# Performance work log

Hardware: AMD Instinct MI355X
Metric: run time of the kernel (lower is better)

Reference implementation:

```python
import jax, jax.numpy as jnp
import numpy as np

B, S, DIM, NH, NKV, HD, HID, L, VOCAB = 1, 2048, 1024, 16, 8, 64, 2816, 2, 32000
EPS = 1e-5
SCALE = float(HD) ** 0.5
NEG = -255.0  # mask fill value used by executorch example inputs


def setup_inputs() -> dict:
    key = jax.random.key(0)
    ks = jax.random.split(key, 16)
    sd = 0.02
    def rnd(k, shape):
        return jax.random.normal(k, shape, dtype=jnp.float32) * sd
    # rope tables: precompute_freqs_cis(head_dim, max_seq_len)[: -1] -> [S, HD//2]
    inv = 1.0 / (10000.0 ** (np.arange(0, HD, 2, dtype=np.float32) / HD))
    ang = np.outer(np.arange(S, dtype=np.float32), inv)
    # causal mask [S, S]
    tril = np.tril(np.ones((S, S), dtype=bool))
    mask = np.where(tril, 0.0, NEG).astype(np.float32)
    return {
        "tokens": jax.random.randint(ks[0], (B, S), 0, VOCAB, dtype=jnp.int32),
        "atten_mask": jnp.asarray(mask),
        "freqs_cos": jnp.asarray(np.cos(ang)),
        "freqs_sin": jnp.asarray(np.sin(ang)),
        "tok_emb": rnd(ks[1], (VOCAB, DIM)),
        "wq": rnd(ks[2], (L, DIM, NH * HD)),
        "wk": rnd(ks[3], (L, DIM, NKV * HD)),
        "wv": rnd(ks[4], (L, DIM, NKV * HD)),
        "wo": rnd(ks[5], (L, NH * HD, DIM)),
        "attn_norm_w": jnp.ones((L, DIM), jnp.float32),
        "ffn_norm_w": jnp.ones((L, DIM), jnp.float32),
        "w1": rnd(ks[6], (L, DIM, HID)),
        "w2": rnd(ks[7], (L, HID, DIM)),
        "w3": rnd(ks[8], (L, DIM, HID)),
        "final_norm_w": jnp.ones((DIM,), jnp.float32),
        "out_w": rnd(ks[9], (DIM, VOCAB)),
    }


def _rmsnorm(x, w):
    return x * jax.lax.rsqrt(jnp.mean(x * x, axis=-1, keepdims=True) + EPS) * w


def _rope(x, c, s):
    # faithful to apply_rotary_emb_single: de-interleave, rotate, concat halves
    xr, xi = x[..., ::2], x[..., 1::2]          # [B,S,H,HD/2]
    c = c[None, :, None, :]
    s = s[None, :, None, :]
    return jnp.concatenate([xr * c - xi * s, xr * s + xi * c], axis=-1)


def reference(tokens, atten_mask, freqs_cos, freqs_sin, tok_emb, wq, wk, wv, wo,
              attn_norm_w, ffn_norm_w, w1, w2, w3, final_norm_w, out_w):
    rep = NH // NKV
    h = tok_emb[tokens]                           # [B,S,DIM]
    k_news, v_news = [], []
    for l in range(L):
        x = _rmsnorm(h, attn_norm_w[l])
        q = (x @ wq[l]).reshape(B, S, NH, HD)
        k = (x @ wk[l]).reshape(B, S, NKV, HD)
        v = (x @ wv[l]).reshape(B, S, NKV, HD)
        q = _rope(q, freqs_cos, freqs_sin)
        k = _rope(k, freqs_cos, freqs_sin)
        # GQA: each kv head serves NH//NKV query heads
        kr = jnp.repeat(k, rep, axis=2)           # [B,S,NH,HD]
        vr = jnp.repeat(v, rep, axis=2)
        attn = jnp.einsum('bshd,bthd->bhst', q, kr) / SCALE + atten_mask[None, None]
        p = jax.nn.softmax(attn, axis=-1)
        y = jnp.einsum('bhst,bthd->bshd', p, vr).reshape(B, S, NH * HD)
        h = h + y @ wo[l]
        x = _rmsnorm(h, ffn_norm_w[l])
        h = h + (jax.nn.silu(x @ w1[l]) * (x @ w3[l])) @ w2[l]
        # output_new_cache_only: last-position rotated K and raw V per kv head
        k_news.append(k[:, -1])                   # [B,NKV,HD]
        v_news.append(v[:, -1])
    logits = _rmsnorm(h, final_norm_w) @ out_w    # [B,S,VOCAB]
    return logits, jnp.stack(k_news), jnp.stack(v_news)
```

## Files before the change

### kernel.cpp

```cpp
#include <hip/hip_runtime.h>
#include <hip/hip_bf16.h>

typedef __bf16 bf16x8 __attribute__((ext_vector_type(8)));
typedef float f32x4 __attribute__((ext_vector_type(4)));
typedef unsigned short ushort4v __attribute__((ext_vector_type(4)));
typedef unsigned short ushort8v __attribute__((ext_vector_type(8)));

#define S_LEN 2048
#define DIM 1024
#define NH 16
#define NKV 8
#define HD 64
#define HID 2816
#define LOGITS ((size_t)S_LEN * 32000)

__device__ __forceinline__ unsigned short f2bf(float f) {
    union { float f; unsigned u; } v; v.f = f;
    unsigned r = v.u + 0x7fffu + ((v.u >> 16) & 1u);
    return (unsigned short)(r >> 16);
}
__device__ __forceinline__ float bf2f(unsigned short u) {
    union { unsigned u; float f; } v; v.u = (unsigned)u << 16; return v.f;
}

__device__ __forceinline__ void gload16(const unsigned short* g, unsigned short* l) {
    __builtin_amdgcn_global_load_lds(
        (const __attribute__((address_space(1))) unsigned int*)g,
        (__attribute__((address_space(3))) unsigned int*)l,
        16, 0, 0);
}

union Frag { f32x4 f; bf16x8 h; };

__device__ __forceinline__ f32x4 lds_read_b128(unsigned addr) {
    f32x4 d;
    asm volatile("ds_read_b128 %0, %1" : "=v"(d) : "v"(addr));
    return d;
}

#define BAR()  asm volatile("s_barrier" ::: "memory")
#define WAITV(n) asm volatile("s_waitcnt vmcnt(" #n ")" ::: "memory")
#define LGKM0() do { asm volatile("s_waitcnt lgkmcnt(0)" ::: "memory"); __builtin_amdgcn_sched_barrier(0); } while (0)

__global__ __launch_bounds__(256) void embed_kernel(const int* __restrict__ tokens,
                                                    const float* __restrict__ emb,
                                                    float* __restrict__ h) {
    int s = blockIdx.x;
    int t = tokens[s];
    float4 v = *(const float4*)&emb[(size_t)t * DIM + threadIdx.x * 4];
    *(float4*)&h[(size_t)s * DIM + threadIdx.x * 4] = v;
}

__global__ __launch_bounds__(256) void rmsnorm_kernel(const float* __restrict__ x,
                                                      const float* __restrict__ w,
                                                      unsigned short* __restrict__ out) {
    __shared__ float sred[4];
    int s = blockIdx.x;
    int tid = threadIdx.x;
    float4 v = *(const float4*)&x[(size_t)s * DIM + tid * 4];
    float ss = v.x * v.x + v.y * v.y + v.z * v.z + v.w * v.w;
#pragma unroll
    for (int off = 32; off; off >>= 1) ss += __shfl_down(ss, off);
    if ((tid & 63) == 0) sred[tid >> 6] = ss;
    __syncthreads();
    float tot = sred[0] + sred[1] + sred[2] + sred[3];
    float scale = rsqrtf(tot * (1.0f / DIM) + 1e-5f);
    float4 wv = *(const float4*)&w[tid * 4];
    ushort4v o;
    o[0] = f2bf(v.x * scale * wv.x); o[1] = f2bf(v.y * scale * wv.y);
    o[2] = f2bf(v.z * scale * wv.z); o[3] = f2bf(v.w * scale * wv.w);
    *(ushort4v*)&out[(size_t)s * DIM + tid * 4] = o;
}

__device__ __forceinline__ void tpose_body(const float* __restrict__ in,
                                           unsigned short* __restrict__ out,
                                           int K, int N, int n0, int k0,
                                           int rowMul, int rowOff) {
    __shared__ unsigned short t[64][68];
    int tid = threadIdx.x;
    int tn = tid & 15, tk = tid >> 4;
#pragma unroll
    for (int p = 0; p < 4; ++p) {
        int k = tk + p * 16;
        float4 v = *(const float4*)&in[(size_t)(k0 + k) * N + n0 + tn * 4];
        t[tn * 4 + 0][k] = f2bf(v.x);
        t[tn * 4 + 1][k] = f2bf(v.y);
        t[tn * 4 + 2][k] = f2bf(v.z);
        t[tn * 4 + 3][k] = f2bf(v.w);
    }
    __syncthreads();
    int wk = tid & 15, wn = tid >> 4;
#pragma unroll
    for (int p = 0; p < 4; ++p) {
        int n = wn + p * 16;
        ushort4v v;
        v[0] = t[n][wk * 4]; v[1] = t[n][wk * 4 + 1];
        v[2] = t[n][wk * 4 + 2]; v[3] = t[n][wk * 4 + 3];
        *(ushort4v*)&out[(size_t)(rowMul * (n0 + n) + rowOff) * K + k0 + wk * 4] = v;
    }
}

__global__ __launch_bounds__(256) void transpose_w(const float* __restrict__ in,
                                                   unsigned short* __restrict__ out,
                                                   int K, int N) {
    tpose_body(in, out, K, N, blockIdx.x * 64, blockIdx.y * 64, 1, 0);
}

__global__ __launch_bounds__(256) void transpose_qkv(const float* __restrict__ wq,
                                                     const float* __restrict__ wk,
                                                     const float* __restrict__ wv,
                                                     unsigned short* __restrict__ out) {
    int z = blockIdx.z;
    if (z > 0 && blockIdx.x >= 8) return;
    const float* in = z == 0 ? wq : (z == 1 ? wk : wv);
    int N = z == 0 ? 1024 : 512;
    int rowOff = z == 0 ? 0 : (z == 1 ? 1024 : 1536);
    tpose_body(in, out, DIM, N, blockIdx.x * 64, blockIdx.y * 64, 1, rowOff);
}

__global__ __launch_bounds__(256) void transpose_w13(const float* __restrict__ w1,
                                                     const float* __restrict__ w3,
                                                     unsigned short* __restrict__ out) {
    int z = blockIdx.z;
    tpose_body(z ? w3 : w1, out, DIM, HID, blockIdx.x * 64, blockIdx.y * 64, 2, z);
}

__global__ __launch_bounds__(256) void transpose_vf(const float* __restrict__ qkvf,
                                                    unsigned short* __restrict__ vT,
                                                    float* __restrict__ out, int layer) {
    __shared__ unsigned short t[64][72];
    int c0 = blockIdx.x * 64, s0 = blockIdx.y * 64;
    int tid = threadIdx.x;
    int tc = tid & 15, ts = tid >> 4;
#pragma unroll
    for (int p = 0; p < 4; ++p) {
        int s = ts + p * 16;
        float4 v = *(const float4*)&qkvf[(size_t)(s0 + s) * 2048 + 1536 + c0 + tc * 4];
        t[tc * 4 + 0][s] = f2bf(v.x);
        t[tc * 4 + 1][s] = f2bf(v.y);
        t[tc * 4 + 2][s] = f2bf(v.z);
        t[tc * 4 + 3][s] = f2bf(v.w);
        if (s0 + s == S_LEN - 1) {
            float* vn = out + LOGITS + 2 * (NKV * HD) + (size_t)layer * (NKV * HD) + c0 + tc * 4;
            vn[0] = v.x; vn[1] = v.y; vn[2] = v.z; vn[3] = v.w;
        }
    }
    __syncthreads();
    int ws_ = tid & 15, wc = tid >> 4;
#pragma unroll
    for (int p = 0; p < 4; ++p) {
        int c = wc + p * 16;
        ushort4v v;
        v[0] = t[c][ws_ * 4]; v[1] = t[c][ws_ * 4 + 1];
        v[2] = t[c][ws_ * 4 + 2]; v[3] = t[c][ws_ * 4 + 3];
        *(ushort4v*)&vT[(size_t)(c0 + c) * 2048 + s0 + ws_ * 4] = v;
    }
}

__global__ __launch_bounds__(256) void gemm_tn(const unsigned short* __restrict__ A, int lda,
                                               const unsigned short* __restrict__ Bt,
                                               float* __restrict__ Cf,
                                               unsigned short* __restrict__ Cb,
                                               const float* __restrict__ addsrc,
                                               int N, int K) {
    __shared__ unsigned short As[128 * 64];
    __shared__ unsigned short Bs[128 * 64];
    int tid = threadIdx.x;
    int lane = tid & 63;
    int wid = tid >> 6;
    int wrow = wid >> 1, wcol = wid & 1;
    int lr = lane & 15, lg = lane >> 4;
    const int m0 = blockIdx.x * 128, n0 = blockIdx.y * 128;

    const int col8 = (((lane & 7) ^ ((lane >> 3) & 7)) * 8);
    const unsigned short* aG = A + (size_t)(m0 + wid * 32 + (lane >> 3)) * lda + col8;
    const unsigned short* bG = Bt + (size_t)(n0 + wid * 32 + (lane >> 3)) * K + col8;
    unsigned short* aL = As + wid * 2048;
    unsigned short* bL = Bs + wid * 2048;

    f32x4 acc[4][4] = {};

    for (int k0 = 0; k0 < K; k0 += 64) {
#pragma unroll
        for (int i = 0; i < 4; ++i)
            gload16(aG + (size_t)(i * 8) * lda + k0, aL + i * 512);
#pragma unroll
        for (int i = 0; i < 4; ++i)
            gload16(bG + (size_t)(i * 8) * K + k0, bL + i * 512);
        __syncthreads();
#pragma unroll
        for (int kk = 0; kk < 2; ++kk) {
            const int slot = ((kk * 4 + lg) ^ (lr & 7)) * 8;
            bf16x8 aF[4], bF[4];
#pragma unroll
            for (int mi = 0; mi < 4; ++mi)
                aF[mi] = *(const bf16x8*)&As[(wrow * 64 + mi * 16 + lr) * 64 + slot];
#pragma unroll
            for (int ni = 0; ni < 4; ++ni)
                bF[ni] = *(const bf16x8*)&Bs[(wcol * 64 + ni * 16 + lr) * 64 + slot];
#pragma unroll
            for (int mi = 0; mi < 4; ++mi)
#pragma unroll
                for (int ni = 0; ni < 4; ++ni)
                    acc[mi][ni] = __builtin_amdgcn_mfma_f32_16x16x32_bf16(aF[mi], bF[ni], acc[mi][ni], 0, 0, 0);
        }
        __syncthreads();
    }
#pragma unroll
    for (int mi = 0; mi < 4; ++mi)
#pragma unroll
        for (int ni = 0; ni < 4; ++ni) {
            int row = m0 + wrow * 64 + mi * 16 + lg * 4;
            int col = n0 + wcol * 64 + ni * 16 + lr;
#pragma unroll
            for (int r = 0; r < 4; ++r) {
                size_t idx = (size_t)(row + r) * N + col;
                float v = acc[mi][ni][r];
                if (addsrc) v += addsrc[idx];
                if (Cb) Cb[idx] = f2bf(v);
                else    Cf[idx] = v;
            }
        }
}

__global__ __launch_bounds__(256) void gemm_tn64(const unsigned short* __restrict__ A, int lda,
                                                 const unsigned short* __restrict__ Bt,
                                                 float* __restrict__ Cf,
                                                 unsigned short* __restrict__ Cb,
                                                 const float* __restrict__ addsrc,
                                                 int N, int K) {
    __shared__ unsigned short As[64 * 64];
    __shared__ unsigned short Bs[128 * 64];
    int tid = threadIdx.x;
    int lane = tid & 63;
    int wid = tid >> 6;
    int lr = lane & 15, lg = lane >> 4;
    const int m0 = blockIdx.x * 64, n0 = blockIdx.y * 128;

    const int srow = tid >> 3;
    const int col8 = (((tid & 7) ^ ((tid >> 3) & 7)) * 8);
    const unsigned short* aG = A + (size_t)(m0 + srow) * lda + col8;
    const unsigned short* bG = Bt + (size_t)(n0 + srow) * K + col8;
    unsigned short* aL = As + wid * 512;
    unsigned short* bL = Bs + wid * 512;

    f32x4 acc[4][2] = {};

    for (int k0 = 0; k0 < K; k0 += 64) {
        gload16(aG + k0, aL);
        gload16(aG + (size_t)32 * lda + k0, aL + 2048);
#pragma unroll
        for (int i = 0; i < 4; ++i)
            gload16(bG + (size_t)(i * 32) * K + k0, bL + i * 2048);
        __syncthreads();
#pragma unroll
        for (int kk = 0; kk < 2; ++kk) {
            const int slot = ((kk * 4 + lg) ^ (lr & 7)) * 8;
            bf16x8 aF[4], bF[2];
#pragma unroll
            for (int mi = 0; mi < 4; ++mi)
                aF[mi] = *(const bf16x8*)&As[(mi * 16 + lr) * 64 + slot];
#pragma unroll
            for (int ni = 0; ni < 2; ++ni)
                bF[ni] = *(const bf16x8*)&Bs[(wid * 32 + ni * 16 + lr) * 64 + slot];
#pragma unroll
            for (int mi = 0; mi < 4; ++mi)
#pragma unroll
                for (int ni = 0; ni < 2; ++ni)
                    acc[mi][ni] = __builtin_amdgcn_mfma_f32_16x16x32_bf16(aF[mi], bF[ni], acc[mi][ni], 0, 0, 0);
        }
        __syncthreads();
    }
#pragma unroll
    for (int mi = 0; mi < 4; ++mi)
#pragma unroll
        for (int ni = 0; ni < 2; ++ni) {
            int row = m0 + mi * 16 + lg * 4;
            int col = n0 + wid * 32 + ni * 16 + lr;
#pragma unroll
            for (int r = 0; r < 4; ++r) {
                size_t idx = (size_t)(row + r) * N + col;
                float v = acc[mi][ni][r];
                if (addsrc) v += addsrc[idx];
                if (Cb) Cb[idx] = f2bf(v);
                else    Cf[idx] = v;
            }
        }
}

template<int FUSE>
__global__ __launch_bounds__(512) void gemm8(const unsigned short* __restrict__ A,
                                             const unsigned short* __restrict__ Bt,
                                             float* __restrict__ Cf,
                                             unsigned short* __restrict__ Cb,
                                             int N, int K) {
    __shared__ unsigned short ldsbuf[65536];
    const int NT = K >> 6;
    int tid = threadIdx.x;
    int lane = tid & 63;
    int wid = tid >> 6;
    int wm = wid >> 2, wn = wid & 3;
    int lr = lane & 15, lg = lane >> 4;
    int wl = blockIdx.x * gridDim.y + blockIdx.y;
    const int m0 = (wl & 7) * 256, n0 = (wl >> 3) * 256;

    unsigned lds0 = (unsigned)(size_t)(__attribute__((address_space(3))) unsigned short*)ldsbuf;
    const unsigned xoff = (unsigned)((lg ^ ((lr >> 1) & 3)) * 16);
    const int gsw = (lane & 3) ^ ((lane >> 3) & 3);
    const int srow = wid * 16 + (lane >> 2);

#define STAGE(buf, ab, s, t) do {                                                   \
        const unsigned short* _src = (ab) ? Bt : A;                                 \
        int _r0 = (ab) ? n0 : m0;                                                   \
        unsigned short* _l = ldsbuf + (((buf) * 2 + (ab)) * 2 + (s)) * 8192 + wid * 512; \
        const unsigned short* _g = _src + (size_t)(_r0 + srow) * K + (size_t)(t) * 64 + (s) * 32 + gsw * 8; \
        gload16(_g, _l);                                                            \
        gload16(_g + (size_t)128 * K, _l + 4096);                                   \
    } while (0)

    f32x4 acc[8][4] = {};

    STAGE(0, 0, 0, 0); STAGE(0, 1, 0, 0);
    STAGE(0, 0, 1, 0); STAGE(0, 1, 1, 0);
    STAGE(1, 0, 0, 1); STAGE(1, 1, 0, 1);
    WAITV(8);
    BAR();

    for (int t = 0; t < NT; ++t) {
        int buf = t & 1;
        unsigned aBase = lds0 + (unsigned)(buf * 65536) + (unsigned)((wm * 128 + lr) * 64) + xoff;
        unsigned bBase = lds0 + (unsigned)(buf * 65536 + 32768) + (unsigned)((wn * 64 + lr) * 64) + xoff;
        Frag aF[4], bF[4];
#pragma unroll
        for (int s = 0; s < 2; ++s) {
#pragma unroll
            for (int ni = 0; ni < 4; ++ni)
                bF[ni].f = lds_read_b128(bBase + (unsigned)(s * 16384 + ni * 1024));
#pragma unroll
            for (int mi = 0; mi < 4; ++mi)
                aF[mi].f = lds_read_b128(aBase + (unsigned)(s * 16384 + mi * 1024));
            if (s == 0) { if (t + 1 < NT) STAGE(buf ^ 1, 0, 1, t + 1); }
            else        { if (t + 2 < NT) STAGE(buf,     0, 0, t + 2); }
            BAR();
            LGKM0();
            __builtin_amdgcn_s_setprio(1);
#pragma unroll
            for (int mi = 0; mi < 4; ++mi)
#pragma unroll
                for (int ni = 0; ni < 4; ++ni)
                    acc[mi][ni] = __builtin_amdgcn_mfma_f32_16x16x32_bf16(aF[mi].h, bF[ni].h, acc[mi][ni], 0, 0, 0);
            __builtin_amdgcn_s_setprio(0);
            BAR();
#pragma unroll
            for (int mi = 0; mi < 4; ++mi)
                aF[mi].f = lds_read_b128(aBase + (unsigned)(4096 + s * 16384 + mi * 1024));
            if (s == 0) { if (t + 1 < NT) STAGE(buf ^ 1, 1, 1, t + 1); }
            else        { if (t + 2 < NT) STAGE(buf,     1, 0, t + 2); }
            BAR();
            LGKM0();
            __builtin_amdgcn_s_setprio(1);
#pragma unroll
            for (int mi = 0; mi < 4; ++mi)
#pragma unroll
                for (int ni = 0; ni < 4; ++ni)
                    acc[4 + mi][ni] = __builtin_amdgcn_mfma_f32_16x16x32_bf16(aF[mi].h, bF[ni].h, acc[4 + mi][ni], 0, 0, 0);
            __builtin_amdgcn_s_setprio(0);
            if (s == 0) {
                if (t + 1 < NT) { WAITV(8); } else { WAITV(0); }
            } else {
                if (t + 2 < NT)      { WAITV(8); }
                else if (t + 1 < NT) { WAITV(4); }
            }
            BAR();
        }
    }
#undef STAGE

#pragma unroll
    for (int mi = 0; mi < 8; ++mi)
#pragma unroll
        for (int ni = 0; ni < 4; ++ni) {
            int row = m0 + wm * 128 + mi * 16 + lg * 4;
            int col = n0 + wn * 64 + ni * 16 + lr;
#pragma unroll
            for (int r = 0; r < 4; ++r) {
                float v = acc[mi][ni][r];
                if (FUSE) {
                    float o = __shfl_xor(v, 1);
                    if (!(lr & 1)) {
                        float res = v / (1.f + __expf(-v)) * o;
                        Cb[(size_t)(row + r) * (HID) + (col >> 1)] = f2bf(res);
                    }
                } else {
                    Cf[(size_t)(row + r) * N + col] = v;
                }
            }
        }
}

__global__ __launch_bounds__(256) void rope_kernel(const float* __restrict__ qkv,
                                                   const float* __restrict__ fc,
                                                   const float* __restrict__ fs,
                                                   unsigned short* __restrict__ qb,
                                                   unsigned short* __restrict__ kb,
                                                   float* __restrict__ out, int layer) {
    int s = blockIdx.x * 4 + (threadIdx.x >> 6);
    int hh = blockIdx.y;
    int lane = threadIdx.x & 63;
    if (lane >= 32) return;
    const float* base = qkv + (size_t)s * 2048;
    if (hh < NH) {
        const float* row = base + hh * HD;
        float2 x2 = *(const float2*)&row[2 * lane];
        float c = fc[s * 32 + lane], sn = fs[s * 32 + lane];
        size_t o = (size_t)s * (NH * HD) + hh * HD + lane;
        qb[o] = f2bf(x2.x * c - x2.y * sn);
        qb[o + 32] = f2bf(x2.x * sn + x2.y * c);
    } else {
        int kh = hh - NH;
        const float* row = base + 1024 + kh * HD;
        float2 x2 = *(const float2*)&row[2 * lane];
        float c = fc[s * 32 + lane], sn = fs[s * 32 + lane];
        float o0 = x2.x * c - x2.y * sn, o1 = x2.x * sn + x2.y * c;
        size_t o = (size_t)s * (NKV * HD) + kh * HD + lane;
        kb[o] = f2bf(o0);
        kb[o + 32] = f2bf(o1);
        if (s == S_LEN - 1) {
            float* kn = out + LOGITS + (size_t)layer * (NKV * HD) + kh * HD;
            kn[lane] = o0; kn[lane + 32] = o1;
        }
    }
}

__global__ __launch_bounds__(256) void attn_kernel(const unsigned short* __restrict__ qb,
                                                   const unsigned short* __restrict__ kb,
                                                   const unsigned short* __restrict__ vT,
                                                   unsigned short* __restrict__ yb) {
    __shared__ unsigned short Klds[2][4096];
    __shared__ unsigned short Vlds[2][4096];
    __shared__ unsigned short P[4][16 * 72];
    int kvh = blockIdx.x;
    int strip = 63 - blockIdx.y;
    int tid = threadIdx.x;
    int lane = tid & 63;
    int w = tid >> 6;
    int hq = w & 1, qsub = w >> 1;
    int h = kvh * 2 + hq;
    int lr = lane & 15, lg = lane >> 4;
    int qbase = strip * 32 + qsub * 16;
    int qrow = qbase + lr;

    const int sr = tid >> 3;
    const int scol8 = (((tid & 7) ^ (sr & 7)) * 8);
    const int NT = (strip >> 1) + 1;

#define STAGEKV(buf, kt) do { \
        gload16(&kb[(size_t)((kt) * 64 + sr) * 512 + kvh * 64 + scol8], &Klds[buf][w * 512]); \
        gload16(&kb[(size_t)((kt) * 64 + sr + 32) * 512 + kvh * 64 + scol8], &Klds[buf][2048 + w * 512]); \
        gload16(&vT[(size_t)(kvh * 64 + sr) * 2048 + (kt) * 64 + scol8], &Vlds[buf][w * 512]); \
        gload16(&vT[(size_t)(kvh * 64 + sr + 32) * 2048 + (kt) * 64 + scol8], &Vlds[buf][2048 + w * 512]); \
    } while (0)

    bf16x8 bq[2];
#pragma unroll
    for (int c = 0; c < 2; ++c)
        bq[c] = *(const bf16x8*)&qb[(size_t)qrow * (NH * HD) + h * HD + c * 32 + lg * 8];

    f32x4 O[4] = {};
    float mstate = -1e30f, lstate = 0.f;

    STAGEKV(0, 0);
    WAITV(0);
    BAR();

    for (int kt = 0; kt < NT; ++kt) {
        int buf = kt & 1;
        if (kt + 1 < NT) STAGEKV(buf ^ 1, kt + 1);
        f32x4 s[4];
#pragma unroll
        for (int kc = 0; kc < 4; ++kc) {
            int krl = kc * 16 + lr;
            const unsigned short* kp = &Klds[buf][krl * 64];
            bf16x8 ak0 = *(const bf16x8*)&kp[((lg ^ (lr & 7)) * 8)];
            bf16x8 ak1 = *(const bf16x8*)&kp[(((4 + lg) ^ (lr & 7)) * 8)];
            f32x4 z = {};
            z = __builtin_amdgcn_mfma_f32_16x16x32_bf16(ak0, bq[0], z, 0, 0, 0);
            z = __builtin_amdgcn_mfma_f32_16x16x32_bf16(ak1, bq[1], z, 0, 0, 0);
            s[kc] = z;
        }
        float tm = -1e30f;
#pragma unroll
        for (int kc = 0; kc < 4; ++kc)
#pragma unroll
            for (int r = 0; r < 4; ++r) {
                int key = kt * 64 + kc * 16 + lg * 4 + r;
                float val = s[kc][r] * 0.125f;
                if (key > qrow) val = -1e30f;
                s[kc][r] = val;
                tm = fmaxf(tm, val);
            }
        tm = fmaxf(tm, __shfl_xor(tm, 16));
        tm = fmaxf(tm, __shfl_xor(tm, 32));
        float mn = fmaxf(mstate, tm);
        float sc = __expf(mstate - mn);
        float rs = 0.f;
        ushort4v pk[4];
#pragma unroll
        for (int kc = 0; kc < 4; ++kc)
#pragma unroll
            for (int r = 0; r < 4; ++r) {
                float pf = __expf(s[kc][r] - mn);
                rs += pf;
                pk[kc][r] = f2bf(pf);
            }
        rs += __shfl_xor(rs, 16);
        rs += __shfl_xor(rs, 32);
        lstate = lstate * sc + rs;
        mstate = mn;
        float osc[4];
#pragma unroll
        for (int r = 0; r < 4; ++r)
            osc[r] = __shfl(sc, lg * 4 + r);
#pragma unroll
        for (int n = 0; n < 4; ++n)
#pragma unroll
            for (int r = 0; r < 4; ++r)
                O[n][r] *= osc[r];
#pragma unroll
        for (int kc = 0; kc < 4; ++kc)
            *(ushort4v*)&P[w][lr * 72 + kc * 16 + lg * 4] = pk[kc];
        bf16x8 pa[2];
#pragma unroll
        for (int g = 0; g < 2; ++g)
            pa[g] = *(const bf16x8*)&P[w][lr * 72 + g * 32 + lg * 8];
#pragma unroll
        for (int n = 0; n < 4; ++n) {
            const unsigned short* vp = &Vlds[buf][(n * 16 + lr) * 64];
#pragma unroll
            for (int g = 0; g < 2; ++g) {
                bf16x8 bv = *(const bf16x8*)&vp[(((g * 4 + lg) ^ (lr & 7)) * 8)];
                O[n] = __builtin_amdgcn_mfma_f32_16x16x32_bf16(pa[g], bv, O[n], 0, 0, 0);
            }
        }
        if (kt + 1 < NT) WAITV(0);
        LGKM0();
        BAR();
    }
#undef STAGEKV

    float linv[4];
#pragma unroll
    for (int r = 0; r < 4; ++r)
        linv[r] = 1.f / __shfl(lstate, lg * 4 + r);
#pragma unroll
    for (int n = 0; n < 4; ++n)
#pragma unroll
        for (int r = 0; r < 4; ++r) {
            int row = qbase + lg * 4 + r;
            yb[(size_t)row * (NH * HD) + h * HD + n * 16 + lr] = f2bf(O[n][r] * linv[r]);
        }
}

extern "C" void kernel_launch(void* const* d_in, const int* in_sizes, int n_in,
                              void* d_out, int out_size, void* d_ws, size_t ws_size,
                              hipStream_t stream) {
    const int* tokens = (const int*)d_in[0];
    const float* freqs_cos = (const float*)d_in[2];
    const float* freqs_sin = (const float*)d_in[3];
    const float* tok_emb = (const float*)d_in[4];
    const float* wq = (const float*)d_in[5];
    const float* wk = (const float*)d_in[6];
    const float* wv = (const float*)d_in[7];
    const float* wo = (const float*)d_in[8];
    const float* attn_norm_w = (const float*)d_in[9];
    const float* ffn_norm_w = (const float*)d_in[10];
    const float* w1 = (const float*)d_in[11];
    const float* w2 = (const float*)d_in[12];
    const float* w3 = (const float*)d_in[13];
    const float* final_norm_w = (const float*)d_in[14];
    const float* out_w = (const float*)d_in[15];
    float* out = (float*)d_out;

    const size_t SD = (size_t)S_LEN * DIM;
    const size_t SKV = (size_t)S_LEN * NKV * HD;

    char* p = (char*)d_ws;
    auto take = [&](size_t bytes) { char* r = p; p += (bytes + 255) & ~(size_t)255; return r; };
    float* h            = (float*)take(SD * 4);
    unsigned short* xnb = (unsigned short*)take(SD * 2);
    char* uni = p;
    float* qkvf         = (float*)uni;
    unsigned short* qb  = (unsigned short*)(uni + 17039360);
    unsigned short* kb  = qb + SD;
    unsigned short* vT  = kb + SKV;
    unsigned short* ybv = vT + SKV;
    unsigned short* gu  = ybv + SD;
    unsigned short* wT  = gu + (size_t)S_LEN * HID;
    unsigned short* owT = (unsigned short*)uni;

    embed_kernel<<<S_LEN, 256, 0, stream>>>(tokens, tok_emb, h);
    for (int l = 0; l < 2; ++l) {
        rmsnorm_kernel<<<S_LEN, 256, 0, stream>>>(h, attn_norm_w + l * DIM, xnb);
        transpose_qkv<<<dim3(16, 16, 3), 256, 0, stream>>>(
            wq + (size_t)l * DIM * 1024, wk + (size_t)l * DIM * 512, wv + (size_t)l * DIM * 512, wT);
        gemm_tn<<<dim3(16, 16), 256, 0, stream>>>(xnb, DIM, wT, qkvf, nullptr, nullptr, 2048, DIM);
        rope_kernel<<<dim3(S_LEN / 4, 24), 256, 0, stream>>>(qkvf, freqs_cos, freqs_sin, qb, kb, out, l);
        transpose_vf<<<dim3(8, 32), 256, 0, stream>>>(qkvf, vT, out, l);
        attn_kernel<<<dim3(NKV, 64), 256, 0, stream>>>(qb, kb, vT, ybv);
        transpose_w<<<dim3(16, 16), 256, 0, stream>>>(wo + (size_t)l * 1024 * DIM, wT, 1024, DIM);
        gemm_tn64<<<dim3(32, 8), 256, 0, stream>>>(ybv, 1024, wT, h, nullptr, h, DIM, 1024);
        rmsnorm_kernel<<<S_LEN, 256, 0, stream>>>(h, ffn_norm_w + l * DIM, xnb);
        transpose_w13<<<dim3(44, 16, 2), 256, 0, stream>>>(
            w1 + (size_t)l * DIM * HID, w3 + (size_t)l * DIM * HID, wT);
        gemm8<1><<<dim3(8, 22), 512, 0, stream>>>(xnb, wT, nullptr, gu, 5632, DIM);
        transpose_w<<<dim3(16, 44), 256, 0, stream>>>(w2 + (size_t)l * HID * 1024, wT, HID, 1024);
        gemm_tn64<<<dim3(32, 8), 256, 0, stream>>>(gu, HID, wT, h, nullptr, h, DIM, HID);
    }
    rmsnorm_kernel<<<S_LEN, 256, 0, stream>>>(h, final_norm_w, xnb);
    transpose_w<<<dim3(500, 16), 256, 0, stream>>>(out_w, owT, DIM, 32000);
    gemm8<0><<<dim3(8, 125), 512, 0, stream>>>(xnb, owT, out, nullptr, 32000, DIM);
}
```

Baseline: 669.5 us.

## Fuse RoPE and V transpose into QKV GEMM epilogue; new K32 output GEMM

The QKV projection GEMM now applies rotary embedding in its epilogue, using a lane shuffle to fetch the paired element. It writes bf16 Q/K and transposed V directly, and stores the last-position K/V cache. This removes the fp32 qkvf intermediate and two extra kernel launches (rope and V transpose). Separately, the final vocab projection switches to a new 256x256-tile GEMM with K-step 32, double-buffered direct global-to-LDS loads and raised wave priority around the MFMA blocks. The epilogue stores are scattered, strided 2-byte writes, which may be less efficient than the old coalesced path.

```diff
diff --git a/kernel.cpp b/kernel.cpp
--- a/kernel.cpp
+++ b/kernel.cpp
@@ -125,46 +125,17 @@
     tpose_body(z ? w3 : w1, out, DIM, HID, blockIdx.x * 64, blockIdx.y * 64, 2, z);
 }
 
-__global__ __launch_bounds__(256) void transpose_vf(const float* __restrict__ qkvf,
-                                                    unsigned short* __restrict__ vT,
-                                                    float* __restrict__ out, int layer) {
-    __shared__ unsigned short t[64][72];
-    int c0 = blockIdx.x * 64, s0 = blockIdx.y * 64;
-    int tid = threadIdx.x;
-    int tc = tid & 15, ts = tid >> 4;
-#pragma unroll
-    for (int p = 0; p < 4; ++p) {
-        int s = ts + p * 16;
-        float4 v = *(const float4*)&qkvf[(size_t)(s0 + s) * 2048 + 1536 + c0 + tc * 4];
-        t[tc * 4 + 0][s] = f2bf(v.x);
-        t[tc * 4 + 1][s] = f2bf(v.y);
-        t[tc * 4 + 2][s] = f2bf(v.z);
-        t[tc * 4 + 3][s] = f2bf(v.w);
-        if (s0 + s == S_LEN - 1) {
-            float* vn = out + LOGITS + 2 * (NKV * HD) + (size_t)layer * (NKV * HD) + c0 + tc * 4;
-            vn[0] = v.x; vn[1] = v.y; vn[2] = v.z; vn[3] = v.w;
-        }
-    }
-    __syncthreads();
-    int ws_ = tid & 15, wc = tid >> 4;
-#pragma unroll
-    for (int p = 0; p < 4; ++p) {
-        int c = wc + p * 16;
-        ushort4v v;
-        v[0] = t[c][ws_ * 4]; v[1] = t[c][ws_ * 4 + 1];
-        v[2] = t[c][ws_ * 4 + 2]; v[3] = t[c][ws_ * 4 + 3];
-        *(ushort4v*)&vT[(size_t)(c0 + c) * 2048 + s0 + ws_ * 4] = v;
-    }
-}
-
-__global__ __launch_bounds__(256) void gemm_tn(const unsigned short* __restrict__ A, int lda,
-                                               const unsigned short* __restrict__ Bt,
-                                               float* __restrict__ Cf,
-                                               unsigned short* __restrict__ Cb,
-                                               const float* __restrict__ addsrc,
-                                               int N, int K) {
+__global__ __launch_bounds__(256) void gemm_qkv(const unsigned short* __restrict__ A,
+                                                const unsigned short* __restrict__ Bt,
+                                                const float* __restrict__ fc,
+                                                const float* __restrict__ fs,
+                                                unsigned short* __restrict__ qb,
+                                                unsigned short* __restrict__ kb,
+                                                unsigned short* __restrict__ vT,
+                                                float* __restrict__ out, int layer) {
     __shared__ unsigned short As[128 * 64];
     __shared__ unsigned short Bs[128 * 64];
+    const int K = DIM, lda = DIM;
     int tid = threadIdx.x;
     int lane = tid & 63;
     int wid = tid >> 6;
@@ -210,15 +181,36 @@
     for (int mi = 0; mi < 4; ++mi)
 #pragma unroll
         for (int ni = 0; ni < 4; ++ni) {
-            int row = m0 + wrow * 64 + mi * 16 + lg * 4;
             int col = n0 + wcol * 64 + ni * 16 + lr;
-#pragma unroll
-            for (int r = 0; r < 4; ++r) {
-                size_t idx = (size_t)(row + r) * N + col;
-                float v = acc[mi][ni][r];
-                if (addsrc) v += addsrc[idx];
-                if (Cb) Cb[idx] = f2bf(v);
-                else    Cf[idx] = v;
+            int s0r = m0 + wrow * 64 + mi * 16 + lg * 4;
+            if (col < 1536) {
+                int p = (col & 63) >> 1;
+                int odd = col & 1;
+#pragma unroll
+                for (int r = 0; r < 4; ++r) {
+                    float v = acc[mi][ni][r];
+                    float o = __shfl_xor(v, 1);
+                    int s = s0r + r;
+                    float c = fc[s * 32 + p], sn = fs[s * 32 + p];
+                    float res = odd ? (o * sn + v * c) : (v * c - o * sn);
+                    int dpos = (odd ? 32 : 0) + p;
+                    if (col < 1024) {
+                        qb[(size_t)s * 1024 + (col >> 6) * 64 + dpos] = f2bf(res);
+                    } else {
+                        int kcol = ((col >> 6) - 16) * 64 + dpos;
+                        kb[(size_t)s * 512 + kcol] = f2bf(res);
+                        if (s == S_LEN - 1)
+                            out[LOGITS + (size_t)layer * 512 + kcol] = res;
+                    }
+                }
+            } else {
+                int d = col - 1536;
+                ushort4v vv;
+#pragma unroll
+                for (int r = 0; r < 4; ++r) vv[r] = f2bf(acc[mi][ni][r]);
+                *(ushort4v*)&vT[(size_t)d * 2048 + s0r] = vv;
+                if (s0r + 3 == S_LEN - 1)
+                    out[LOGITS + 2 * 512 + (size_t)layer * 512 + d] = acc[mi][ni][3];
             }
         }
 }
@@ -226,7 +218,6 @@
 __global__ __launch_bounds__(256) void gemm_tn64(const unsigned short* __restrict__ A, int lda,
                                                  const unsigned short* __restrict__ Bt,
                                                  float* __restrict__ Cf,
-                                                 unsigned short* __restrict__ Cb,
                                                  const float* __restrict__ addsrc,
                                                  int N, int K) {
     __shared__ unsigned short As[64 * 64];
@@ -282,8 +273,7 @@
                 size_t idx = (size_t)(row + r) * N + col;
                 float v = acc[mi][ni][r];
                 if (addsrc) v += addsrc[idx];
-                if (Cb) Cb[idx] = f2bf(v);
-                else    Cf[idx] = v;
+                Cf[idx] = v;
             }
         }
 }
@@ -398,38 +388,96 @@
         }
 }
 
-__global__ __launch_bounds__(256) void rope_kernel(const float* __restrict__ qkv,
-                                                   const float* __restrict__ fc,
-                                                   const float* __restrict__ fs,
-                                                   unsigned short* __restrict__ qb,
-                                                   unsigned short* __restrict__ kb,
-                                                   float* __restrict__ out, int layer) {
-    int s = blockIdx.x * 4 + (threadIdx.x >> 6);
-    int hh = blockIdx.y;
-    int lane = threadIdx.x & 63;
-    if (lane >= 32) return;
-    const float* base = qkv + (size_t)s * 2048;
-    if (hh < NH) {
-        const float* row = base + hh * HD;
-        float2 x2 = *(const float2*)&row[2 * lane];
-        float c = fc[s * 32 + lane], sn = fs[s * 32 + lane];
-        size_t o = (size_t)s * (NH * HD) + hh * HD + lane;
-        qb[o] = f2bf(x2.x * c - x2.y * sn);
-        qb[o + 32] = f2bf(x2.x * sn + x2.y * c);
-    } else {
-        int kh = hh - NH;
-        const float* row = base + 1024 + kh * HD;
-        float2 x2 = *(const float2*)&row[2 * lane];
-        float c = fc[s * 32 + lane], sn = fs[s * 32 + lane];
-        float o0 = x2.x * c - x2.y * sn, o1 = x2.x * sn + x2.y * c;
-        size_t o = (size_t)s * (NKV * HD) + kh * HD + lane;
-        kb[o] = f2bf(o0);
-        kb[o + 32] = f2bf(o1);
-        if (s == S_LEN - 1) {
-            float* kn = out + LOGITS + (size_t)layer * (NKV * HD) + kh * HD;
-            kn[lane] = o0; kn[lane + 32] = o1;
-        }
-    }
+__global__ __launch_bounds__(512) void gemm8k32(const unsigned short* __restrict__ A,
+                                                const unsigned short* __restrict__ Bt,
+                                                float* __restrict__ Cf,
+                                                int N, int K) {
+    __shared__ unsigned short ldsbuf[32768];
+    const int NT = K >> 5;
+    int tid = threadIdx.x;
+    int lane = tid & 63;
+    int wid = tid >> 6;
+    int wm = wid >> 2, wn = wid & 3;
+    int lr = lane & 15, lg = lane >> 4;
+    int wl = blockIdx.x * gridDim.y + blockIdx.y;
+    const int m0 = (wl & 7) * 256, n0 = (wl >> 3) * 256;
+
+    unsigned lds0 = (unsigned)(size_t)(__attribute__((address_space(3))) unsigned short*)ldsbuf;
+    const unsigned xoff = (unsigned)((lg ^ ((lr >> 1) & 3)) * 16);
+    const int gsw = (lane & 3) ^ ((lane >> 3) & 3);
+    const int srow = wid * 16 + (lane >> 2);
+
+#define STGA(t) do { \
+        unsigned short* _l = ldsbuf + (((t) & 1) * 2 + 0) * 8192 + wid * 512; \
+        const unsigned short* _g = A + (size_t)(m0 + srow) * K + (size_t)(t) * 32 + gsw * 8; \
+        gload16(_g, _l); \
+        gload16(_g + (size_t)128 * K, _l + 4096); \
+    } while (0)
+#define STGB(t) do { \
+        unsigned short* _l = ldsbuf + (((t) & 1) * 2 + 1) * 8192 + wid * 512; \
+        const unsigned short* _g = Bt + (size_t)(n0 + srow) * K + (size_t)(t) * 32 + gsw * 8; \
+        gload16(_g, _l); \
+        gload16(_g + (size_t)128 * K, _l + 4096); \
+    } while (0)
+
+    f32x4 acc[8][4] = {};
+
+    STGA(0); STGB(0); STGB(1);
+    WAITV(2);
+    BAR();
+
+    for (int t = 0; t < NT; ++t) {
+        int buf = t & 1;
+        unsigned aBase = lds0 + (unsigned)(buf * 32768) + (unsigned)((wm * 128 + lr) * 64) + xoff;
+        unsigned bBase = lds0 + (unsigned)(buf * 32768 + 16384) + (unsigned)((wn * 64 + lr) * 64) + xoff;
+        Frag aF[4], bF[4];
+#pragma unroll
+        for (int ni = 0; ni < 4; ++ni)
+            bF[ni].f = lds_read_b128(bBase + (unsigned)(ni * 1024));
+#pragma unroll
+        for (int mi = 0; mi < 4; ++mi)
+            aF[mi].f = lds_read_b128(aBase + (unsigned)(mi * 1024));
+        if (t + 1 < NT) STGA(t + 1);
+        BAR();
+        LGKM0();
+        __builtin_amdgcn_s_setprio(1);
+#pragma unroll
+        for (int mi = 0; mi < 4; ++mi)
+#pragma unroll
+            for (int ni = 0; ni < 4; ++ni)
+                acc[mi][ni] = __builtin_amdgcn_mfma_f32_16x16x32_bf16(aF[mi].h, bF[ni].h, acc[mi][ni], 0, 0, 0);
+        __builtin_amdgcn_s_setprio(0);
+        BAR();
+#pragma unroll
+        for (int mi = 0; mi < 4; ++mi)
+            aF[mi].f = lds_read_b128(aBase + (unsigned)(4096 + mi * 1024));
+        if (t + 2 < NT) STGB(t + 2);
+        BAR();
+        LGKM0();
+        __builtin_amdgcn_s_setprio(1);
+#pragma unroll
+        for (int mi = 0; mi < 4; ++mi)
+#pragma unroll
+            for (int ni = 0; ni < 4; ++ni)
+                acc[4 + mi][ni] = __builtin_amdgcn_mfma_f32_16x16x32_bf16(aF[mi].h, bF[ni].h, acc[4 + mi][ni], 0, 0, 0);
+        __builtin_amdgcn_s_setprio(0);
+        if (t + 2 < NT)      { WAITV(2); }
+        else if (t + 1 < NT) { WAITV(0); }
+        BAR();
+    }
+#undef STGA
+#undef STGB
+
+#pragma unroll
+    for (int mi = 0; mi < 8; ++mi)
+#pragma unroll
+        for (int ni = 0; ni < 4; ++ni) {
+            int row = m0 + wm * 128 + mi * 16 + lg * 4;
+            int col = n0 + wn * 64 + ni * 16 + lr;
+#pragma unroll
+            for (int r = 0; r < 4; ++r)
+                Cf[(size_t)(row + r) * N + col] = acc[mi][ni][r];
+        }
 }
 
 __global__ __launch_bounds__(256) void attn_kernel(const unsigned short* __restrict__ qb,
@@ -589,8 +637,7 @@
     float* h            = (float*)take(SD * 4);
     unsigned short* xnb = (unsigned short*)take(SD * 2);
     char* uni = p;
-    float* qkvf         = (float*)uni;
-    unsigned short* qb  = (unsigned short*)(uni + 17039360);
+    unsigned short* qb  = (unsigned short*)uni;
     unsigned short* kb  = qb + SD;
     unsigned short* vT  = kb + SKV;
     unsigned short* ybv = vT + SKV;
@@ -603,20 +650,19 @@
         rmsnorm_kernel<<<S_LEN, 256, 0, stream>>>(h, attn_norm_w + l * DIM, xnb);
         transpose_qkv<<<dim3(16, 16, 3), 256, 0, stream>>>(
             wq + (size_t)l * DIM * 1024, wk + (size_t)l * DIM * 512, wv + (size_t)l * DIM * 512, wT);
-        gemm_tn<<<dim3(16, 16), 256, 0, stream>>>(xnb, DIM, wT, qkvf, nullptr, nullptr, 2048, DIM);
-        rope_kernel<<<dim3(S_LEN / 4, 24), 256, 0, stream>>>(qkvf, freqs_cos, freqs_sin, qb, kb, out, l);
-        transpose_vf<<<dim3(8, 32), 256, 0, stream>>>(qkvf, vT, out, l);
+        gemm_qkv<<<dim3(16, 16), 256, 0, stream>>>(xnb, wT, freqs_cos, freqs_sin,
+                                                   qb, kb, vT, out, l);
         attn_kernel<<<dim3(NKV, 64), 256, 0, stream>>>(qb, kb, vT, ybv);
         transpose_w<<<dim3(16, 16), 256, 0, stream>>>(wo + (size_t)l * 1024 * DIM, wT, 1024, DIM);
-        gemm_tn64<<<dim3(32, 8), 256, 0, stream>>>(ybv, 1024, wT, h, nullptr, h, DIM, 1024);
+        gemm_tn64<<<dim3(32, 8), 256, 0, stream>>>(ybv, 1024, wT, h, h, DIM, 1024);
         rmsnorm_kernel<<<S_LEN, 256, 0, stream>>>(h, ffn_norm_w + l * DIM, xnb);
         transpose_w13<<<dim3(44, 16, 2), 256, 0, stream>>>(
             w1 + (size_t)l * DIM * HID, w3 + (size_t)l * DIM * HID, wT);
         gemm8<1><<<dim3(8, 22), 512, 0, stream>>>(xnb, wT, nullptr, gu, 5632, DIM);
         transpose_w<<<dim3(16, 44), 256, 0, stream>>>(w2 + (size_t)l * HID * 1024, wT, HID, 1024);
-        gemm_tn64<<<dim3(32, 8), 256, 0, stream>>>(gu, HID, wT, h, nullptr, h, DIM, HID);
+        gemm_tn64<<<dim3(32, 8), 256, 0, stream>>>(gu, HID, wT, h, h, DIM, HID);
     }
     rmsnorm_kernel<<<S_LEN, 256, 0, stream>>>(h, final_norm_w, xnb);
     transpose_w<<<dim3(500, 16), 256, 0, stream>>>(out_w, owT, DIM, 32000);
-    gemm8<0><<<dim3(8, 125), 512, 0, stream>>>(xnb, owT, out, nullptr, 32000, DIM);
-}
+    gemm8k32<<<dim3(8, 125), 512, 0, stream>>>(xnb, owT, out, 32000, DIM);
+}
```

New measurement: 648.2 us (median of 2 runs). 3.2% less time.
